# Optimization experiments

Measured on AMD Instinct MI355X. Metric: run time of the kernel, lower is better.

## Reference

```python
import jax, jax.numpy as jnp
import numpy as np

IN_F = 8192
OUT_F = 8192
BATCH = 16

def setup_inputs() -> dict:
    key = jax.random.key(0)
    k_x, k_q, k_s, k_b = jax.random.split(key, 4)
    x = jax.random.normal(k_x, (BATCH, IN_F), dtype=jnp.float32)
    # symmetric int4: values in [-8, 7]
    qweight = jax.random.randint(k_q, (OUT_F, IN_F), -8, 8, dtype=jnp.int32)
    scale = jax.random.uniform(k_s, (), dtype=jnp.float32) * 0.05 + 1e-3
    bias = jax.random.normal(k_b, (OUT_F,), dtype=jnp.float32)
    return {"x": x, "qweight": qweight, "scale": scale, "bias": bias}

def reference(x, qweight, scale, bias):
    # F.linear(x, qweight.float() * scale, bias)
    # Factor scale out of the GEMM: (x @ (q*s).T) == (x @ q.T) * s
    acc = jnp.einsum('bi,oi->bo', x, qweight.astype(jnp.float32))
    return acc * scale + bias
```

## Files before the change

kernel.cpp:

```cpp
#include <hip/hip_runtime.h>
#include <hip/hip_bf16.h>

#define IN_F  8192
#define OUT_F 8192
#define BATCH 16
#define KSPLIT 8
#define KCHUNK (IN_F / KSPLIT)
#define NSTEPS (KCHUNK / 32)
#define THREADS 256
#define ROWS_PER_BLOCK 64
#define XPAD 8
#define XSTRIDE (KCHUNK + XPAD)
#define WS_NEEDED ((size_t)KSPLIT * BATCH * OUT_F * 4)

typedef __attribute__((ext_vector_type(8))) short bf16x8;
typedef __attribute__((ext_vector_type(4))) float f32x4;

__global__ __launch_bounds__(256)
void init_out_kernel(const float* __restrict__ bias, float* __restrict__ out)
{
    const int i = blockIdx.x * 256 + threadIdx.x;
    out[i] = bias[i & (OUT_F - 1)];
}

__global__ __launch_bounds__(256)
void reduce_kernel(const float* __restrict__ ws,
                   const float* __restrict__ scale,
                   const float* __restrict__ bias,
                   float* __restrict__ out)
{
    const int idx = (blockIdx.x * 256 + threadIdx.x) * 4;
    const int o   = idx & (OUT_F - 1);
    float4 s = {0.f, 0.f, 0.f, 0.f};
    #pragma unroll
    for (int k = 0; k < KSPLIT; ++k) {
        const float4 p = *reinterpret_cast<const float4*>(ws + (size_t)k * BATCH * OUT_F + idx);
        s.x += p.x; s.y += p.y; s.z += p.z; s.w += p.w;
    }
    const float sc = scale[0];
    const float4 bv = *reinterpret_cast<const float4*>(bias + o);
    float4 r;
    r.x = s.x * sc + bv.x; r.y = s.y * sc + bv.y;
    r.z = s.z * sc + bv.z; r.w = s.w * sc + bv.w;
    *reinterpret_cast<float4*>(out + idx) = r;
}

template<bool USE_WS>
__global__ __launch_bounds__(THREADS, 4)
void gptq_mfma_kernel(const float* __restrict__ x,
                      const int*  __restrict__ qw,
                      const float* __restrict__ scale,
                      float* __restrict__ dst)
{
    __shared__ __align__(16) unsigned short xs[BATCH][XSTRIDE];

    const int tid  = threadIdx.x;
    const int lane = tid & 63;
    const int wave = tid >> 6;
    const int mn   = lane & 15;
    const int kgrp = lane >> 4;
    const int kidx = blockIdx.x & (KSPLIT - 1);
    const int row0 = (blockIdx.x >> 3) * ROWS_PER_BLOCK + wave * 16;
    const int k0   = kidx * KCHUNK;

    #pragma unroll
    for (int r = 0; r < BATCH; ++r) {
        const float4 v = *reinterpret_cast<const float4*>(x + (size_t)r * IN_F + k0 + tid * 4);
        ushort4 p;
        p.x = __bfloat16_as_ushort(__float2bfloat16(v.x));
        p.y = __bfloat16_as_ushort(__float2bfloat16(v.y));
        p.z = __bfloat16_as_ushort(__float2bfloat16(v.z));
        p.w = __bfloat16_as_ushort(__float2bfloat16(v.w));
        *reinterpret_cast<ushort4*>(&xs[r][tid * 4]) = p;
    }
    __syncthreads();

    const int* qsrc = qw + (size_t)(row0 + mn) * IN_F + k0 + kgrp * 8;
    const unsigned short* asrc = &xs[mn][kgrp * 8];

    f32x4 acc = {0.f, 0.f, 0.f, 0.f};

    int4 c0a = *reinterpret_cast<const int4*>(qsrc);
    int4 c0b = *reinterpret_cast<const int4*>(qsrc + 4);
    bf16x8 a0 = *reinterpret_cast<const bf16x8*>(asrc);
    int4 c1a = *reinterpret_cast<const int4*>(qsrc + 32);
    int4 c1b = *reinterpret_cast<const int4*>(qsrc + 36);
    bf16x8 a1 = *reinterpret_cast<const bf16x8*>(asrc + 32);

    #pragma unroll 1
    for (int s = 0; s < NSTEPS; s += 2) {
        int4 n0a, n0b, n1a, n1b;
        bf16x8 na0, na1;
        const bool m0 = (s + 2 < NSTEPS);
        const bool m1 = (s + 3 < NSTEPS);
        if (m0) {
            n0a = *reinterpret_cast<const int4*>(qsrc + (s + 2) * 32);
            n0b = *reinterpret_cast<const int4*>(qsrc + (s + 2) * 32 + 4);
            na0 = *reinterpret_cast<const bf16x8*>(asrc + (s + 2) * 32);
        }
        if (m1) {
            n1a = *reinterpret_cast<const int4*>(qsrc + (s + 3) * 32);
            n1b = *reinterpret_cast<const int4*>(qsrc + (s + 3) * 32 + 4);
            na1 = *reinterpret_cast<const bf16x8*>(asrc + (s + 3) * 32);
        }

        bf16x8 bw;
        bw[0] = __bfloat16_as_short(__float2bfloat16((float)c0a.x));
        bw[1] = __bfloat16_as_short(__float2bfloat16((float)c0a.y));
        bw[2] = __bfloat16_as_short(__float2bfloat16((float)c0a.z));
        bw[3] = __bfloat16_as_short(__float2bfloat16((float)c0a.w));
        bw[4] = __bfloat16_as_short(__float2bfloat16((float)c0b.x));
        bw[5] = __bfloat16_as_short(__float2bfloat16((float)c0b.y));
        bw[6] = __bfloat16_as_short(__float2bfloat16((float)c0b.z));
        bw[7] = __bfloat16_as_short(__float2bfloat16((float)c0b.w));
        acc = __builtin_amdgcn_mfma_f32_16x16x32_bf16(a0, bw, acc, 0, 0, 0);

        bw[0] = __bfloat16_as_short(__float2bfloat16((float)c1a.x));
        bw[1] = __bfloat16_as_short(__float2bfloat16((float)c1a.y));
        bw[2] = __bfloat16_as_short(__float2bfloat16((float)c1a.z));
        bw[3] = __bfloat16_as_short(__float2bfloat16((float)c1a.w));
        bw[4] = __bfloat16_as_short(__float2bfloat16((float)c1b.x));
        bw[5] = __bfloat16_as_short(__float2bfloat16((float)c1b.y));
        bw[6] = __bfloat16_as_short(__float2bfloat16((float)c1b.z));
        bw[7] = __bfloat16_as_short(__float2bfloat16((float)c1b.w));
        acc = __builtin_amdgcn_mfma_f32_16x16x32_bf16(a1, bw, acc, 0, 0, 0);

        if (m0) { c0a = n0a; c0b = n0b; a0 = na0; }
        if (m1) { c1a = n1a; c1b = n1b; a1 = na1; }
    }

    const float sc = scale[0];
    #pragma unroll
    for (int v = 0; v < 4; ++v) {
        const int m = kgrp * 4 + v;
        if (USE_WS) {
            dst[(size_t)kidx * BATCH * OUT_F + (size_t)m * OUT_F + row0 + mn] = acc[v];
        } else {
            atomicAdd(dst + (size_t)m * OUT_F + row0 + mn, acc[v] * sc);
        }
    }
}

extern "C" void kernel_launch(void* const* d_in, const int* in_sizes, int n_in,
                              void* d_out, int out_size, void* d_ws, size_t ws_size,
                              hipStream_t stream) {
    const float* x     = (const float*)d_in[0];
    const int*   qw    = (const int*)d_in[1];
    const float* scale = (const float*)d_in[2];
    const float* bias  = (const float*)d_in[3];
    float*       out   = (float*)d_out;
    float*       ws    = (float*)d_ws;

    dim3 grid((OUT_F / ROWS_PER_BLOCK) * KSPLIT);

    if (ws_size >= WS_NEEDED) {
        gptq_mfma_kernel<true><<<grid, THREADS, 0, stream>>>(x, qw, scale, ws);
        reduce_kernel<<<(BATCH * OUT_F) / 4 / 256, 256, 0, stream>>>(ws, scale, bias, out);
    } else {
        init_out_kernel<<<(BATCH * OUT_F) / 256, 256, 0, stream>>>(bias, out);
        gptq_mfma_kernel<false><<<grid, THREADS, 0, stream>>>(x, qw, scale, out);
    }
}
```

Measured before the change: 52.65 us.

## Double K-split, raise occupancy, and issue first weight load before x staging

Raises KSPLIT from 8 to 16, halving each block's K chunk so the grid doubles and the LDS x tile shrinks. Launch bounds are raised to 8 blocks per CU, and the main loop's prefetch depth drops from two steps to one to save registers. The first weight loads are now issued before x is staged into LDS so their latency overlaps the staging. The trade-offs are a larger workspace and reduce pass (16 partials) and less in-flight memory per wave, which the higher occupancy is meant to make up for.

New measurement: 51.59 us. -2.0%, faster.

```diff
diff --git a/kernel.cpp b/kernel.cpp
--- a/kernel.cpp
+++ b/kernel.cpp
@@ -4,7 +4,7 @@
 #define IN_F  8192
 #define OUT_F 8192
 #define BATCH 16
-#define KSPLIT 8
+#define KSPLIT 16
 #define KCHUNK (IN_F / KSPLIT)
 #define NSTEPS (KCHUNK / 32)
 #define THREADS 256
@@ -46,7 +46,7 @@
 }
 
 template<bool USE_WS>
-__global__ __launch_bounds__(THREADS, 4)
+__global__ __launch_bounds__(THREADS, 8)
 void gptq_mfma_kernel(const float* __restrict__ x,
                       const int*  __restrict__ qw,
                       const float* __restrict__ scale,
@@ -60,73 +60,52 @@
     const int mn   = lane & 15;
     const int kgrp = lane >> 4;
     const int kidx = blockIdx.x & (KSPLIT - 1);
-    const int row0 = (blockIdx.x >> 3) * ROWS_PER_BLOCK + wave * 16;
+    const int row0 = (blockIdx.x >> 4) * ROWS_PER_BLOCK + wave * 16;
     const int k0   = kidx * KCHUNK;
+
+    const int* qsrc = qw + (size_t)(row0 + mn) * IN_F + k0 + kgrp * 8;
+
+    int4 ca = *reinterpret_cast<const int4*>(qsrc);
+    int4 cb = *reinterpret_cast<const int4*>(qsrc + 4);
 
     #pragma unroll
     for (int r = 0; r < BATCH; ++r) {
-        const float4 v = *reinterpret_cast<const float4*>(x + (size_t)r * IN_F + k0 + tid * 4);
-        ushort4 p;
-        p.x = __bfloat16_as_ushort(__float2bfloat16(v.x));
-        p.y = __bfloat16_as_ushort(__float2bfloat16(v.y));
-        p.z = __bfloat16_as_ushort(__float2bfloat16(v.z));
-        p.w = __bfloat16_as_ushort(__float2bfloat16(v.w));
-        *reinterpret_cast<ushort4*>(&xs[r][tid * 4]) = p;
+        const float2 v = *reinterpret_cast<const float2*>(x + (size_t)r * IN_F + k0 + tid * 2);
+        unsigned int p = (__bfloat16_as_ushort(__float2bfloat16(v.y)) << 16)
+                       |  __bfloat16_as_ushort(__float2bfloat16(v.x));
+        *reinterpret_cast<unsigned int*>(&xs[r][tid * 2]) = p;
     }
     __syncthreads();
 
-    const int* qsrc = qw + (size_t)(row0 + mn) * IN_F + k0 + kgrp * 8;
     const unsigned short* asrc = &xs[mn][kgrp * 8];
+    bf16x8 ac = *reinterpret_cast<const bf16x8*>(asrc);
 
     f32x4 acc = {0.f, 0.f, 0.f, 0.f};
 
-    int4 c0a = *reinterpret_cast<const int4*>(qsrc);
-    int4 c0b = *reinterpret_cast<const int4*>(qsrc + 4);
-    bf16x8 a0 = *reinterpret_cast<const bf16x8*>(asrc);
-    int4 c1a = *reinterpret_cast<const int4*>(qsrc + 32);
-    int4 c1b = *reinterpret_cast<const int4*>(qsrc + 36);
-    bf16x8 a1 = *reinterpret_cast<const bf16x8*>(asrc + 32);
-
     #pragma unroll 1
-    for (int s = 0; s < NSTEPS; s += 2) {
-        int4 n0a, n0b, n1a, n1b;
-        bf16x8 na0, na1;
-        const bool m0 = (s + 2 < NSTEPS);
-        const bool m1 = (s + 3 < NSTEPS);
-        if (m0) {
-            n0a = *reinterpret_cast<const int4*>(qsrc + (s + 2) * 32);
-            n0b = *reinterpret_cast<const int4*>(qsrc + (s + 2) * 32 + 4);
-            na0 = *reinterpret_cast<const bf16x8*>(asrc + (s + 2) * 32);
-        }
-        if (m1) {
-            n1a = *reinterpret_cast<const int4*>(qsrc + (s + 3) * 32);
-            n1b = *reinterpret_cast<const int4*>(qsrc + (s + 3) * 32 + 4);
-            na1 = *reinterpret_cast<const bf16x8*>(asrc + (s + 3) * 32);
+    for (int s = 0; s < NSTEPS; ++s) {
+        int4 na, nb;
+        bf16x8 an;
+        const bool more = (s + 1 < NSTEPS);
+        if (more) {
+            na = *reinterpret_cast<const int4*>(qsrc + (s + 1) * 32);
+            nb = *reinterpret_cast<const int4*>(qsrc + (s + 1) * 32 + 4);
+            an = *reinterpret_cast<const bf16x8*>(asrc + (s + 1) * 32);
         }
 
         bf16x8 bw;
-        bw[0] = __bfloat16_as_short(__float2bfloat16((float)c0a.x));
-        bw[1] = __bfloat16_as_short(__float2bfloat16((float)c0a.y));
-        bw[2] = __bfloat16_as_short(__float2bfloat16((float)c0a.z));
-        bw[3] = __bfloat16_as_short(__float2bfloat16((float)c0a.w));
-        bw[4] = __bfloat16_as_short(__float2bfloat16((float)c0b.x));
-        bw[5] = __bfloat16_as_short(__float2bfloat16((float)c0b.y));
-        bw[6] = __bfloat16_as_short(__float2bfloat16((float)c0b.z));
-        bw[7] = __bfloat16_as_short(__float2bfloat16((float)c0b.w));
-        acc = __builtin_amdgcn_mfma_f32_16x16x32_bf16(a0, bw, acc, 0, 0, 0);
+        bw[0] = __bfloat16_as_short(__float2bfloat16((float)ca.x));
+        bw[1] = __bfloat16_as_short(__float2bfloat16((float)ca.y));
+        bw[2] = __bfloat16_as_short(__float2bfloat16((float)ca.z));
+        bw[3] = __bfloat16_as_short(__float2bfloat16((float)ca.w));
+        bw[4] = __bfloat16_as_short(__float2bfloat16((float)cb.x));
+        bw[5] = __bfloat16_as_short(__float2bfloat16((float)cb.y));
+        bw[6] = __bfloat16_as_short(__float2bfloat16((float)cb.z));
+        bw[7] = __bfloat16_as_short(__float2bfloat16((float)cb.w));
 
-        bw[0] = __bfloat16_as_short(__float2bfloat16((float)c1a.x));
-        bw[1] = __bfloat16_as_short(__float2bfloat16((float)c1a.y));
-        bw[2] = __bfloat16_as_short(__float2bfloat16((float)c1a.z));
-        bw[3] = __bfloat16_as_short(__float2bfloat16((float)c1a.w));
-        bw[4] = __bfloat16_as_short(__float2bfloat16((float)c1b.x));
-        bw[5] = __bfloat16_as_short(__float2bfloat16((float)c1b.y));
-        bw[6] = __bfloat16_as_short(__float2bfloat16((float)c1b.z));
-        bw[7] = __bfloat16_as_short(__float2bfloat16((float)c1b.w));
-        acc = __builtin_amdgcn_mfma_f32_16x16x32_bf16(a1, bw, acc, 0, 0, 0);
+        acc = __builtin_amdgcn_mfma_f32_16x16x32_bf16(ac, bw, acc, 0, 0, 0);
 
-        if (m0) { c0a = n0a; c0b = n0b; a0 = na0; }
-        if (m1) { c1a = n1a; c1b = n1b; a1 = na1; }
+        if (more) { ca = na; cb = nb; ac = an; }
     }
 
     const float sc = scale[0];
```
